# Kernel tuning notes

Measured on AMD Instinct MI355X. Metric: run time of the kernel, lower is better.

## Reference

```python
import jax, jax.numpy as jnp
import numpy as np

B, C, N = 8, 64, 4096
K, M = 20, 8  # neighbors, num_kernel
OUT_C = 64
NEG_SLOPE = 0.2


def setup_inputs() -> dict:
    key = jax.random.key(0)
    k1, k2, k3, k4, k5, k6 = jax.random.split(key, 6)
    x = jax.random.normal(k1, (B, 3, N), dtype=jnp.float32)
    feature = jax.random.normal(k2, (B, C, N), dtype=jnp.float32)
    neigh_indexs = jax.random.randint(k3, (B, N, K), 0, N, dtype=jnp.int64)
    kernels = jax.random.normal(k4, (3, M), dtype=jnp.float32)
    conv_w = jax.random.normal(k5, (OUT_C, C * M), dtype=jnp.float32) * (1.0 / np.sqrt(C * M))
    conv_b = jax.random.normal(k6, (OUT_C,), dtype=jnp.float32) * 0.01
    return {"x": x, "feature": feature, "neigh_indexs": neigh_indexs,
            "kernels": kernels, "conv_w": conv_w, "conv_b": conv_b}


def reference(x, feature, neigh_indexs, kernels, conv_w, conv_b):
    b, c, n = feature.shape
    k = K
    m = kernels.shape[1]
    idx = neigh_indexs[:, :, :k]  # dilation=1 slice, (B,N,K)
    bidx = jnp.arange(b)[:, None, None]

    xt = jnp.transpose(x, (0, 2, 1))            # (B,N,3)
    x_neighs = xt[bidx, idx]                    # (B,N,K,3) irregular gather
    x_rel = x_neighs - x_neighs[:, :, :1, :]    # relative coords to first neighbor

    # kernel projection + one_padding buffer (zeros with [0,0]=1)
    one_pad = jnp.zeros((k, m), dtype=x.dtype).at[0, 0].set(1.0)
    permatrix = jnp.einsum('bnkc,cm->bnkm', x_rel, kernels) + one_pad
    # topkmax: stable softmax over the neighbor axis (soft assignment of
    # neighbors to each of the m kernel slots)
    permatrix = jax.nn.softmax(permatrix, axis=2)  # (B,N,K,M)

    ft = jnp.transpose(feature, (0, 2, 1))      # (B,N,C)
    f_neighs = ft[bidx, idx]                    # (B,N,K,C)
    # feats (B*N,C,K) @ permatrix (B*N,K,M) -> (B*N,C,M); flatten C-major
    agg = jnp.einsum('bnkc,bnkm->bncm', f_neighs, permatrix).reshape(b, n, c * m)

    # BasicConv: 1x1 conv == dense over channel dim, then LeakyReLU(0.2)
    out = agg @ conv_w.T + conv_b               # (B,N,out_c)
    out = jax.nn.leaky_relu(out, NEG_SLOPE)
    out = jnp.transpose(out, (0, 2, 1))         # (B,out_c,N)
    return out + feature                        # residual since in_c == out_c
```

## Files before the change

kernel.cpp:

```cpp
#include <hip/hip_runtime.h>

#define BB 8
#define CC 64
#define NNN 4096
#define KK 20
#define MM 8
#define OC 64
#define CM 512

typedef __attribute__((ext_vector_type(8))) short bf16x8;
typedef __attribute__((ext_vector_type(4))) float f32x4;

__device__ __forceinline__ unsigned short f2bf(float f) {
    union { float f; unsigned int u; } v; v.f = f;
    unsigned int u = v.u;
    return (unsigned short)((u + 0x7FFFu + ((u >> 16) & 1u)) >> 16);
}
__device__ __forceinline__ float bfhi2f(unsigned int u) {
    union { unsigned int u; float f; } v; v.u = u & 0xffff0000u; return v.f;
}
__device__ __forceinline__ float bflo2f(unsigned int u) {
    union { unsigned int u; float f; } v; v.u = u << 16; return v.f;
}

#if __has_builtin(__builtin_amdgcn_fdot2_f32_bf16)
typedef __attribute__((ext_vector_type(2))) __bf16 bf16x2_t;
__device__ __forceinline__ float dot2bf(unsigned int a, unsigned int b, float c) {
    union { unsigned int u; bf16x2_t v; } ua, ub; ua.u = a; ub.u = b;
    return __builtin_amdgcn_fdot2_f32_bf16(ua.v, ub.v, c, false);
}
#else
__device__ __forceinline__ float dot2bf(unsigned int a, unsigned int b, float c) {
    float d;
    asm("v_dot2_f32_bf16 %0, %1, %2, %3" : "=v"(d) : "v"(a), "v"(b), "v"(c));
    return d;
}
#endif

__global__ __launch_bounds__(256) void prep_kernel(const float* __restrict__ feature,
                                                   const float* __restrict__ conv_w,
                                                   unsigned short* __restrict__ ftr,
                                                   unsigned short* __restrict__ Wb) {
    int blk = blockIdx.x;
    int t = threadIdx.x;
    if (blk < 512) {
        __shared__ float tile[64 * 65];
        int b = blk & 7;
        int n0 = (blk >> 3) << 6;
        const float* fb = feature + b * (CC * NNN);
        #pragma unroll
        for (int s = 0; s < 16; ++s) {
            int i = t + s * 256;
            int c = i >> 6, nn = i & 63;
            tile[c * 65 + nn] = fb[c * NNN + n0 + nn];
        }
        __syncthreads();
        unsigned short* fo = ftr + b * (NNN * CC) + n0 * CC;
        #pragma unroll
        for (int s = 0; s < 16; ++s) {
            int i = t + s * 256;
            int n = i >> 6, cc = i & 63;
            fo[n * CC + cc] = f2bf(tile[cc * 65 + n]);
        }
    } else {
        int base = (blk - 512) * 8192;
        #pragma unroll
        for (int s = 0; s < 32; ++s) {
            int i = base + t + s * 256;
            Wb[i] = f2bf(conv_w[i]);
        }
    }
}

__global__ __launch_bounds__(256, 4) void main_kernel(
    const float* __restrict__ x,
    const float* __restrict__ feature,
    const int* __restrict__ nidx,
    const float* __restrict__ kern,
    const float* __restrict__ conv_b,
    const unsigned short* __restrict__ ftr,
    const unsigned short* __restrict__ Wb,
    float* __restrict__ out)
{
    __shared__ __align__(16) union {
        struct {
            int   idx[16 * KK];
            float xn[16 * KK * 3];
            unsigned int permb[16 * 10 * MM];
        } s;
        unsigned short aggA[16 * 520];
    } u;

    int t = threadIdx.x;
    int blk = blockIdx.x;
    int b = blk & 7;
    int n0 = (blk >> 3) << 4;
    int w = t >> 6, l = t & 63;

    int o = (w << 4) + (l & 15);
    int pq = (l >> 4) << 2;
    float4 fres4 = *(const float4*)(feature + ((size_t)b * CC + o) * NNN + n0 + pq);
    float bias = conv_b[o];
    int m_pre = t & 7;
    float kw0 = kern[m_pre], kw1 = kern[MM + m_pre], kw2 = kern[2 * MM + m_pre];

    const int* nb = nidx + (b * NNN + n0) * KK;
    for (int i = t; i < 16 * KK; i += 256) u.s.idx[i] = nb[i];
    __syncthreads();

    const float* xb = x + b * (3 * NNN);
    float xreg[4];
    int xslot[4];
    #pragma unroll
    for (int s = 0; s < 4; ++s) {
        int i = t + s * 256;
        xslot[s] = i;
        if (i < 960) {
            int p2 = i / 60;
            int rem = i - p2 * 60;
            int k = rem / 3;
            int c = rem - k * 3;
            xreg[s] = xb[c * NNN + u.s.idx[p2 * KK + k]];
        }
    }

    int p = t >> 4;
    int cq = (t & 15) << 2;
    const unsigned short* fb = ftr + (size_t)b * (NNN * CC);
    uint2 fr[KK];
    #pragma unroll
    for (int k = 0; k < KK; ++k)
        fr[k] = *(const uint2*)(fb + (size_t)u.s.idx[p * KK + k] * CC + cq);

    #pragma unroll
    for (int s = 0; s < 4; ++s)
        if (xslot[s] < 960) u.s.xn[xslot[s]] = xreg[s];
    __syncthreads();

    if (t < 128) {
        int pp = t >> 3;
        int m = t & 7;
        const float* xp = &u.s.xn[pp * 60];
        float bx = xp[0], by = xp[1], bz = xp[2];
        float pv[KK];
        #pragma unroll
        for (int k = 0; k < KK; ++k) {
            float dx = xp[k * 3 + 0] - bx;
            float dy = xp[k * 3 + 1] - by;
            float dz = xp[k * 3 + 2] - bz;
            pv[k] = dx * kw0 + dy * kw1 + dz * kw2;
        }
        if (m == 0) pv[0] += 1.0f;
        float mx = pv[0];
        #pragma unroll
        for (int k = 1; k < KK; ++k) mx = fmaxf(mx, pv[k]);
        float sum = 0.f;
        #pragma unroll
        for (int k = 0; k < KK; ++k) { pv[k] = __expf(pv[k] - mx); sum += pv[k]; }
        float inv = 1.0f / sum;
        #pragma unroll
        for (int i = 0; i < 10; ++i) {
            unsigned int lo = f2bf(pv[2 * i] * inv);
            unsigned int hi = f2bf(pv[2 * i + 1] * inv);
            u.s.permb[(pp * 10 + i) * MM + m] = lo | (hi << 16);
        }
    }
    __syncthreads();

    float acc[4][MM];
    #pragma unroll
    for (int ci = 0; ci < 4; ++ci)
        #pragma unroll
        for (int m = 0; m < MM; ++m) acc[ci][m] = 0.f;

    const unsigned int* pb = &u.s.permb[p * 10 * MM];
    #pragma unroll
    for (int i = 0; i < 10; ++i) {
        uint4 pm0 = *(const uint4*)(pb + i * MM);
        uint4 pm1 = *(const uint4*)(pb + i * MM + 4);
        unsigned int fp0 = __builtin_amdgcn_perm(fr[2 * i + 1].x, fr[2 * i].x, 0x05040100u);
        unsigned int fp1 = __builtin_amdgcn_perm(fr[2 * i + 1].x, fr[2 * i].x, 0x07060302u);
        unsigned int fp2 = __builtin_amdgcn_perm(fr[2 * i + 1].y, fr[2 * i].y, 0x05040100u);
        unsigned int fp3 = __builtin_amdgcn_perm(fr[2 * i + 1].y, fr[2 * i].y, 0x07060302u);
        unsigned int fpv[4] = {fp0, fp1, fp2, fp3};
        unsigned int pmv[8] = {pm0.x, pm0.y, pm0.z, pm0.w, pm1.x, pm1.y, pm1.z, pm1.w};
        #pragma unroll
        for (int ci = 0; ci < 4; ++ci)
            #pragma unroll
            for (int m = 0; m < MM; ++m)
                acc[ci][m] = dot2bf(fpv[ci], pmv[m], acc[ci][m]);
    }
    __syncthreads();

    #pragma unroll
    for (int ci = 0; ci < 4; ++ci) {
        union { bf16x8 v; unsigned short s2[8]; } pk;
        #pragma unroll
        for (int m = 0; m < MM; ++m) pk.s2[m] = f2bf(acc[ci][m]);
        *(bf16x8*)&u.aggA[p * 520 + (cq + ci) * MM] = pk.v;
    }
    __syncthreads();

    {
        int row = l & 15;
        int kg = (l >> 4) << 3;
        f32x4 acc2 = {0.f, 0.f, 0.f, 0.f};
        const unsigned short* wrow = Wb + (size_t)o * CM;
        const unsigned short* arow = u.aggA + row * 520;
        #pragma unroll
        for (int s = 0; s < 16; ++s) {
            int k = s * 32 + kg;
            bf16x8 af = *(const bf16x8*)&arow[k];
            bf16x8 bfr = *(const bf16x8*)&wrow[k];
            acc2 = __builtin_amdgcn_mfma_f32_16x16x32_bf16(af, bfr, acc2, 0, 0, 0);
        }
        float4 res;
        #pragma unroll
        for (int r = 0; r < 4; ++r) {
            float v = acc2[r] + bias;
            v = v > 0.f ? v : v * 0.2f;
            ((float*)&res)[r] = v + ((const float*)&fres4)[r];
        }
        *(float4*)(out + ((size_t)b * CC + o) * NNN + n0 + pq) = res;
    }
}

extern "C" void kernel_launch(void* const* d_in, const int* in_sizes, int n_in,
                              void* d_out, int out_size, void* d_ws, size_t ws_size,
                              hipStream_t stream) {
    const float* x        = (const float*)d_in[0];
    const float* feature  = (const float*)d_in[1];
    const int*   nidx     = (const int*)d_in[2];
    const float* kern     = (const float*)d_in[3];
    const float* conv_w   = (const float*)d_in[4];
    const float* conv_b   = (const float*)d_in[5];
    float* out = (float*)d_out;

    unsigned short* ftr = (unsigned short*)d_ws;
    unsigned short* Wb  = (unsigned short*)((char*)d_ws + 4194304);

    prep_kernel<<<516, 256, 0, stream>>>(feature, conv_w, ftr, Wb);
    main_kernel<<<2048, 256, 0, stream>>>(x, feature, nidx, kern, conv_b, ftr, Wb, out);
}
```

Before: 105.2 us.

## Process 32 points per block with 512 threads and separate LDS buffers

```diff
diff --git a/kernel.cpp b/kernel.cpp
--- a/kernel.cpp
+++ b/kernel.cpp
@@ -1,4 +1,5 @@
 #include <hip/hip_runtime.h>
+#include <hip/hip_bf16.h>
 
 #define BB 8
 #define CC 64
@@ -7,14 +8,15 @@
 #define MM 8
 #define OC 64
 #define CM 512
+#define PTS 32
 
 typedef __attribute__((ext_vector_type(8))) short bf16x8;
 typedef __attribute__((ext_vector_type(4))) float f32x4;
 
 __device__ __forceinline__ unsigned short f2bf(float f) {
-    union { float f; unsigned int u; } v; v.f = f;
-    unsigned int u = v.u;
-    return (unsigned short)((u + 0x7FFFu + ((u >> 16) & 1u)) >> 16);
+    union { __hip_bfloat16 h; unsigned short s; } v;
+    v.h = __float2bfloat16(f);
+    return v.s;
 }
 __device__ __forceinline__ float bfhi2f(unsigned int u) {
     union { unsigned int u; float f; } v; v.u = u & 0xffff0000u; return v.f;
@@ -72,7 +74,7 @@
     }
 }
 
-__global__ __launch_bounds__(256, 4) void main_kernel(
+__global__ __launch_bounds__(512, 4) void main_kernel(
     const float* __restrict__ x,
     const float* __restrict__ feature,
     const int* __restrict__ nidx,
@@ -82,46 +84,45 @@
     const unsigned short* __restrict__ Wb,
     float* __restrict__ out)
 {
-    __shared__ __align__(16) union {
-        struct {
-            int   idx[16 * KK];
-            float xn[16 * KK * 3];
-            unsigned int permb[16 * 10 * MM];
-        } s;
-        unsigned short aggA[16 * 520];
-    } u;
+    __shared__ __align__(16) struct {
+        int   idx[PTS * KK];
+        float xn[PTS * 64];
+        unsigned int permb[PTS * 10 * MM];
+    } s;
+    __shared__ __align__(16) unsigned short aggA[PTS * 520];
 
     int t = threadIdx.x;
     int blk = blockIdx.x;
     int b = blk & 7;
-    int n0 = (blk >> 3) << 4;
+    int n0 = (blk >> 3) << 5;
     int w = t >> 6, l = t & 63;
 
-    int o = (w << 4) + (l & 15);
-    int pq = (l >> 4) << 2;
+    int o = ((w & 3) << 4) + (l & 15);
+    int pg = (w >> 2) << 4;
+    int pq = pg + ((l >> 4) << 2);
     float4 fres4 = *(const float4*)(feature + ((size_t)b * CC + o) * NNN + n0 + pq);
     float bias = conv_b[o];
     int m_pre = t & 7;
     float kw0 = kern[m_pre], kw1 = kern[MM + m_pre], kw2 = kern[2 * MM + m_pre];
 
     const int* nb = nidx + (b * NNN + n0) * KK;
-    for (int i = t; i < 16 * KK; i += 256) u.s.idx[i] = nb[i];
+    for (int i = t; i < PTS * KK; i += 512) s.idx[i] = nb[i];
     __syncthreads();
 
     const float* xb = x + b * (3 * NNN);
     float xreg[4];
     int xslot[4];
     #pragma unroll
-    for (int s = 0; s < 4; ++s) {
-        int i = t + s * 256;
-        xslot[s] = i;
-        if (i < 960) {
+    for (int sI = 0; sI < 4; ++sI) {
+        int i = t + sI * 512;
+        if (i < PTS * KK * 3) {
             int p2 = i / 60;
             int rem = i - p2 * 60;
             int k = rem / 3;
             int c = rem - k * 3;
-            xreg[s] = xb[c * NNN + u.s.idx[p2 * KK + k]];
-        }
+            xslot[sI] = p2 * 64 + rem;
+            xreg[sI] = xb[c * NNN + s.idx[p2 * KK + k]];
+        } else xslot[sI] = -1;
     }
 
     int p = t >> 4;
@@ -130,17 +131,17 @@
     uint2 fr[KK];
     #pragma unroll
     for (int k = 0; k < KK; ++k)
-        fr[k] = *(const uint2*)(fb + (size_t)u.s.idx[p * KK + k] * CC + cq);
-
-    #pragma unroll
-    for (int s = 0; s < 4; ++s)
-        if (xslot[s] < 960) u.s.xn[xslot[s]] = xreg[s];
-    __syncthreads();
-
-    if (t < 128) {
+        fr[k] = *(const uint2*)(fb + (size_t)s.idx[p * KK + k] * CC + cq);
+
+    #pragma unroll
+    for (int sI = 0; sI < 4; ++sI)
+        if (xslot[sI] >= 0) s.xn[xslot[sI]] = xreg[sI];
+    __syncthreads();
+
+    if (t < 256) {
         int pp = t >> 3;
         int m = t & 7;
-        const float* xp = &u.s.xn[pp * 60];
+        const float* xp = &s.xn[pp * 64];
         float bx = xp[0], by = xp[1], bz = xp[2];
         float pv[KK];
         #pragma unroll
@@ -162,7 +163,7 @@
         for (int i = 0; i < 10; ++i) {
             unsigned int lo = f2bf(pv[2 * i] * inv);
             unsigned int hi = f2bf(pv[2 * i + 1] * inv);
-            u.s.permb[(pp * 10 + i) * MM + m] = lo | (hi << 16);
+            s.permb[(pp * 10 + i) * MM + m] = lo | (hi << 16);
         }
     }
     __syncthreads();
@@ -173,7 +174,7 @@
         #pragma unroll
         for (int m = 0; m < MM; ++m) acc[ci][m] = 0.f;
 
-    const unsigned int* pb = &u.s.permb[p * 10 * MM];
+    const unsigned int* pb = &s.permb[p * 10 * MM];
     #pragma unroll
     for (int i = 0; i < 10; ++i) {
         uint4 pm0 = *(const uint4*)(pb + i * MM);
@@ -190,14 +191,13 @@
             for (int m = 0; m < MM; ++m)
                 acc[ci][m] = dot2bf(fpv[ci], pmv[m], acc[ci][m]);
     }
-    __syncthreads();
 
     #pragma unroll
     for (int ci = 0; ci < 4; ++ci) {
         union { bf16x8 v; unsigned short s2[8]; } pk;
         #pragma unroll
         for (int m = 0; m < MM; ++m) pk.s2[m] = f2bf(acc[ci][m]);
-        *(bf16x8*)&u.aggA[p * 520 + (cq + ci) * MM] = pk.v;
+        *(bf16x8*)&aggA[p * 520 + (cq + ci) * MM] = pk.v;
     }
     __syncthreads();
 
@@ -206,10 +206,10 @@
         int kg = (l >> 4) << 3;
         f32x4 acc2 = {0.f, 0.f, 0.f, 0.f};
         const unsigned short* wrow = Wb + (size_t)o * CM;
-        const unsigned short* arow = u.aggA + row * 520;
-        #pragma unroll
-        for (int s = 0; s < 16; ++s) {
-            int k = s * 32 + kg;
+        const unsigned short* arow = aggA + (size_t)(pg + row) * 520;
+        #pragma unroll
+        for (int sI = 0; sI < 16; ++sI) {
+            int k = sI * 32 + kg;
             bf16x8 af = *(const bf16x8*)&arow[k];
             bf16x8 bfr = *(const bf16x8*)&wrow[k];
             acc2 = __builtin_amdgcn_mfma_f32_16x16x32_bf16(af, bfr, acc2, 0, 0, 0);
@@ -240,5 +240,5 @@
     unsigned short* Wb  = (unsigned short*)((char*)d_ws + 4194304);
 
     prep_kernel<<<516, 256, 0, stream>>>(feature, conv_w, ftr, Wb);
-    main_kernel<<<2048, 256, 0, stream>>>(x, feature, nidx, kern, conv_b, ftr, Wb, out);
-}
+    main_kernel<<<1024, 512, 0, stream>>>(x, feature, nidx, kern, conv_b, ftr, Wb, out);
+}
```

New measurement: 109.8 us. +4.4%, slower.
